# Kernel tuning notes

Measured on AMD Instinct MI355X. Metric: run time of the kernel, lower is better.

Reference implementation:

```python
import jax, jax.numpy as jnp
import numpy as np

I, C, H, W = 8, 32, 240, 320
GX = GY = GZ = 64


def setup_inputs() -> dict:
    key = jax.random.key(0)
    k_img, = jax.random.split(key, 1)
    images = jax.random.normal(k_img, (I, C, H, W), dtype=jnp.float32)

    # Camera intrinsics (shared across views)
    fx = fy = 300.0
    cx, cy = (W - 1) / 2.0, (H - 1) / 2.0
    K = jnp.array([[fx, 0.0, cx], [0.0, fy, cy], [0.0, 0.0, 1.0]], dtype=jnp.float32)

    # World->camera extrinsics: identity rotation, cameras spread along x
    centers = jnp.stack(
        [jnp.linspace(-0.175, 0.175, I), jnp.zeros(I), jnp.zeros(I)], axis=1
    ).astype(jnp.float32)  # [I,3] camera centers in world
    Rm = jnp.broadcast_to(jnp.eye(3, dtype=jnp.float32), (I, 3, 3))
    t = -jnp.einsum('iab,ib->ia', Rm, centers)  # t = -R c
    T_cw = jnp.concatenate(
        [jnp.concatenate([Rm, t[:, :, None]], axis=2),
         jnp.broadcast_to(jnp.array([[0.0, 0.0, 0.0, 1.0]], dtype=jnp.float32), (I, 1, 4))],
        axis=1,
    )  # [I,4,4]
    transformations = jnp.einsum('ab,ibc->iac', K, T_cw[:, :3, :])  # [I,3,4]

    # Voxel grid of world coordinates in front of the cameras
    xs = jnp.linspace(-1.0, 1.0, GX)
    ys = jnp.linspace(-1.0, 1.0, GY)
    zs = jnp.linspace(1.5, 3.5, GZ)
    gx, gy, gz = jnp.meshgrid(xs, ys, zs, indexing='ij')
    coordinates = jnp.stack([gx, gy, gz], axis=0).astype(jnp.float32)  # [3,X,Y,Z]

    return {
        'images': images,
        'transformations': transformations,
        'T_cw': T_cw,
        'coordinates': coordinates,
    }


def reference(images, transformations, T_cw, coordinates):
    # images: [I,C,H,W]; transformations: [I,3,4]; T_cw: [I,4,4]; coordinates: [3,X,Y,Z]
    Ii, Cc, Hh, Ww = images.shape
    X, Y, Z = coordinates.shape[1:]
    pts = coordinates.reshape(3, -1)  # [3, N]
    N = pts.shape[1]
    ph = jnp.concatenate([pts, jnp.ones((1, N), pts.dtype)], axis=0)  # [4, N]

    # Camera-frame depth
    cam = jnp.einsum('iab,bn->ian', T_cw[:, :3, :], ph)  # [I,3,N]
    depth = cam[:, 2, :]  # [I,N]

    # Pixel projection
    proj = jnp.einsum('iab,bn->ian', transformations, ph)  # [I,3,N]
    wz = proj[:, 2, :]
    wz_safe = jnp.where(jnp.abs(wz) < 1e-8, 1e-8, wz)
    u = proj[:, 0, :] / wz_safe
    v = proj[:, 1, :] / wz_safe

    valid = (u >= 0) & (u <= Ww - 1) & (v >= 0) & (v <= Hh - 1) & (depth > 0)
    validf = valid.astype(images.dtype)  # [I,N]

    # Nearest-neighbor grid sampling (grid_sampling_mode='nearest')
    ui = jnp.clip(jnp.round(u), 0, Ww - 1).astype(jnp.int32)
    vi = jnp.clip(jnp.round(v), 0, Hh - 1).astype(jnp.int32)
    feats = jax.vmap(lambda img, vv, uu: img[:, vv, uu])(images, vi, ui)  # [I,C,N]
    feats = feats * validf[:, None, :]

    # Viewing direction: normalized ray from camera center to voxel
    Rm = T_cw[:, :3, :3]
    t = T_cw[:, :3, 3]
    centers = -jnp.einsum('iba,ib->ia', Rm, t)  # R^T t -> camera centers [I,3]
    d = pts[None, :, :] - centers[:, :, None]  # [I,3,N]
    d = d / (jnp.linalg.norm(d, axis=1, keepdims=True) + 1e-8)

    # Concatenate channels: features + projected depth + validity + view dir
    grid = jnp.concatenate(
        [feats, depth[:, None, :], validf[:, None, :], d], axis=1
    )  # [I, C+5, N]
    grid = grid.reshape(Ii, Cc + 5, X, Y, Z)
    return grid, coordinates
```

## Files before the change

kernel.cpp:

```cpp
#include <hip/hip_runtime.h>
#include <stdint.h>


constexpr int I_ = 8;
constexpr int C_ = 32;
constexpr int H_ = 240;
constexpr int W_ = 320;
constexpr int HW_ = H_ * W_;
constexpr int N_ = 1 << 18;
constexpr int OUTC_ = 37;

constexpr int GZT    = 16;
constexpr int ROWF   = 328;
constexpr int ROWB   = ROWF * 4;
constexpr int STAGEB = GZT * ROWB;
constexpr int NCHUNK = 21;
constexpr int BUFF   = NCHUNK * 256;
constexpr uint32_t PLANEB = HW_ * 4;

typedef __attribute__((address_space(3))) uint8_t       as3_b;
typedef __attribute__((address_space(1))) const uint8_t as1_b;

struct Proj { float u, v, depth; bool valid; };

__device__ __forceinline__ Proj project(const float* __restrict__ P,
                                        const float* __restrict__ T,
                                        float x, float y, float z) {
    Proj r;
    r.depth = T[8]*x + T[9]*y + T[10]*z + T[11];
    const float px = P[0]*x + P[1]*y + P[2]*z  + P[3];
    const float py = P[4]*x + P[5]*y + P[6]*z  + P[7];
    const float pz = P[8]*x + P[9]*y + P[10]*z + P[11];
    const float wz = (fabsf(pz) < 1e-8f) ? 1e-8f : pz;
    r.u = px / wz;
    r.v = py / wz;
    r.valid = (r.u >= 0.0f) && (r.u <= (float)(W_-1)) &&
              (r.v >= 0.0f) && (r.v <= (float)(H_-1)) && (r.depth > 0.0f);
    return r;
}

__global__ __launch_bounds__(256) void smear_stage(
    const float* __restrict__ images,
    const float* __restrict__ trans,
    const float* __restrict__ T_cw,
    const float* __restrict__ coords,
    float* __restrict__ out)
{
    __shared__ float xs[64];
    __shared__ float zs[GZT];
    __shared__ float yv;
    __shared__ int   rowv[GZT];
    __shared__ alignas(16) float stagef[2][BUFF];

    const int cpx = (int)gridDim.x >> 3;
    const int bid = ((int)blockIdx.x & 7) * cpx + ((int)blockIdx.x >> 3);
    const int i  = bid >> 8;
    const int gy = (bid >> 2) & 63;
    const int zg = bid & 3;
    const int nbase = gy * 64 + zg * GZT;

    const int t = (int)threadIdx.x;
    const int w = t >> 6;
    const int lane = t & 63;

    if (t < 64)            xs[t]      = coords[(size_t)t * 4096 + nbase];
    else if (t < 64 + GZT) zs[t - 64] = coords[2 * N_ + nbase + (t - 64)];
    else if (t == 80)      yv         = coords[N_ + nbase];
    __syncthreads();

    const float* P = trans + i * 12;
    const float* T = T_cw + i * 16;
    const float y = yv;

    if (t < GZT) {
        Proj p0 = project(P, T, xs[0], y, zs[t]);
        rowv[t] = (int)fminf(fmaxf(rintf(p0.v), 0.0f), (float)(H_-1));
    }
    __syncthreads();

    const int gx = t >> 2;
    const int j0 = (t & 3) * 4;
    const float x = xs[gx];

    int   lofsf[4];
    float vf[4];
    int ok = 1;
    #pragma unroll
    for (int j = 0; j < 4; ++j) {
        const int s = j0 + j;
        Proj pr = project(P, T, x, y, zs[s]);
        const int ui = (int)fminf(fmaxf(rintf(pr.u), 0.0f), (float)(W_-1));
        const int vi = (int)fminf(fmaxf(rintf(pr.v), 0.0f), (float)(H_-1));
        vf[j]    = pr.valid ? 1.0f : 0.0f;
        lofsf[j] = s * ROWF + ui;
        ok &= ((vi == rowv[s]) || !pr.valid) ? 1 : 0;
    }
    const int blockok = __syncthreads_and(ok);

    float* optr = out + (size_t)i * OUTC_ * N_ + nbase + (size_t)gx * 4096 + j0;
    const uint8_t* img_i = (const uint8_t*)(images + (size_t)i * C_ * HW_);

    if (blockok) {
        uint32_t coff[6];
        #pragma unroll
        for (int q = 0; q < 6; ++q) {
            const int qg = w + 4 * q;
            coff[q] = 0;
            if (qg < NCHUNK) {
                const int p = qg * 1024 + lane * 16;
                int s = p / ROWB; if (s > GZT - 1) s = GZT - 1;
                const int off = p - s * ROWB;
                uint32_t ro = (uint32_t)(rowv[s] * (W_ * 4) + off);
                const uint32_t lim = PLANEB - 16;
                coff[q] = ro < lim ? ro : lim;
            }
        }

        #pragma unroll
        for (int q = 0; q < 6; ++q) {
            const int qg = w + 4 * q;
            if (qg < NCHUNK)
                __builtin_amdgcn_global_load_lds(
                    (const as1_b*)(img_i + coff[q]),
                    (as3_b*)&stagef[0][qg * 256], 16, 0, 0);
        }
        __syncthreads();

        float4 pend;
        for (int c = 0; c < C_; ++c) {
            if (c) *(float4*)(optr + (size_t)(c - 1) * N_) = pend;
            if (c + 1 < C_) {
                const uint8_t* plane = img_i + (size_t)(c + 1) * PLANEB;
                float* dstb = stagef[(c + 1) & 1];
                #pragma unroll
                for (int q = 0; q < 6; ++q) {
                    const int qg = w + 4 * q;
                    if (qg < NCHUNK)
                        __builtin_amdgcn_global_load_lds(
                            (const as1_b*)(plane + coff[q]),
                            (as3_b*)&dstb[qg * 256], 16, 0, 0);
                }
            }
            const float* bb = stagef[c & 1];
            const float g0 = bb[lofsf[0]] * vf[0];
            const float g1 = bb[lofsf[1]] * vf[1];
            const float g2 = bb[lofsf[2]] * vf[2];
            const float g3 = bb[lofsf[3]] * vf[3];
            pend = make_float4(g0, g1, g2, g3);
            __syncthreads();
        }
        *(float4*)(optr + (size_t)(C_ - 1) * N_) = pend;
    } else {
        for (int c = 0; c < C_; ++c) {
            const float* plane = (const float*)img_i + (size_t)c * HW_;
            float g[4];
            #pragma unroll
            for (int j = 0; j < 4; ++j) {
                const int s = j0 + j;
                Proj pr = project(P, T, x, y, zs[s]);
                const int ui = (int)fminf(fmaxf(rintf(pr.u), 0.0f), (float)(W_-1));
                const int vi = (int)fminf(fmaxf(rintf(pr.v), 0.0f), (float)(H_-1));
                g[j] = pr.valid ? plane[vi * W_ + ui] : 0.0f;
            }
            *(float4*)(optr + (size_t)c * N_) = make_float4(g[0], g[1], g[2], g[3]);
        }
    }

    const float cxx = -(T[0]*T[3] + T[4]*T[7] + T[8] *T[11]);
    const float cyy = -(T[1]*T[3] + T[5]*T[7] + T[9] *T[11]);
    const float czz = -(T[2]*T[3] + T[6]*T[7] + T[10]*T[11]);
    float dep[4], dxn[4], dyn[4], dzn[4];
    #pragma unroll
    for (int j = 0; j < 4; ++j) {
        const int s = j0 + j;
        const float z = zs[s];
        Proj pr = project(P, T, x, y, z);
        dep[j] = pr.depth;
        vf[j]  = pr.valid ? 1.0f : 0.0f;
        const float dx = x - cxx, dy = y - cyy, dz = z - czz;
        const float inv = 1.0f / (sqrtf(dx*dx + dy*dy + dz*dz) + 1e-8f);
        dxn[j] = dx * inv; dyn[j] = dy * inv; dzn[j] = dz * inv;
    }
    *(float4*)(optr + (size_t)32 * N_) = make_float4(dep[0], dep[1], dep[2], dep[3]);
    *(float4*)(optr + (size_t)33 * N_) = make_float4(vf[0],  vf[1],  vf[2],  vf[3]);
    *(float4*)(optr + (size_t)34 * N_) = make_float4(dxn[0], dxn[1], dxn[2], dxn[3]);
    *(float4*)(optr + (size_t)35 * N_) = make_float4(dyn[0], dyn[1], dyn[2], dyn[3]);
    *(float4*)(optr + (size_t)36 * N_) = make_float4(dzn[0], dzn[1], dzn[2], dzn[3]);
}

extern "C" void kernel_launch(void* const* d_in, const int* in_sizes, int n_in,
                              void* d_out, int out_size, void* d_ws, size_t ws_size,
                              hipStream_t stream) {
    const float* images = (const float*)d_in[0];
    const float* trans  = (const float*)d_in[1];
    const float* T_cw   = (const float*)d_in[2];
    const float* coords = (const float*)d_in[3];
    float* out = (float*)d_out;

    smear_stage<<<I_ * 64 * 4, 256, 0, stream>>>(images, trans, T_cw, coords, out);

    float* coords_out = out + (size_t)I_ * OUTC_ * N_;
    hipMemcpyAsync(coords_out, coords, (size_t)3 * N_ * sizeof(float),
                   hipMemcpyDeviceToDevice, stream);
}
```

Baseline: 482.4 us.

## Split channels into groups across blocks and use nontemporal output stores

Each block now handles 8 of the 32 channels, so the grid grows fourfold. This adds parallelism and shortens each block's serial channel loop. The block-to-view mapping changes so that consecutive blocks cover different views, which is likely aimed at XCD/L2 locality. Output stores become nontemporal to avoid cache pollution. The trade-off is that projection setup and the row-check are repeated in each channel group. The depth, validity and view-direction channels are written only by group 0.

```diff
diff --git a/kernel.cpp b/kernel.cpp
--- a/kernel.cpp
+++ b/kernel.cpp
@@ -4,22 +4,29 @@
 
 constexpr int I_ = 8;
 constexpr int C_ = 32;
+constexpr int W_ = 320;
 constexpr int H_ = 240;
-constexpr int W_ = 320;
 constexpr int HW_ = H_ * W_;
 constexpr int N_ = 1 << 18;
 constexpr int OUTC_ = 37;
+constexpr int CPG_ = 8;
+constexpr int NCG_ = C_ / CPG_;
 
 constexpr int GZT    = 16;
 constexpr int ROWF   = 328;
 constexpr int ROWB   = ROWF * 4;
-constexpr int STAGEB = GZT * ROWB;
 constexpr int NCHUNK = 21;
 constexpr int BUFF   = NCHUNK * 256;
 constexpr uint32_t PLANEB = HW_ * 4;
 
 typedef __attribute__((address_space(3))) uint8_t       as3_b;
 typedef __attribute__((address_space(1))) const uint8_t as1_b;
+typedef float f32x4 __attribute__((ext_vector_type(4)));
+
+__device__ __forceinline__ void ntstore4(float* p, float a, float b, float c, float d) {
+    f32x4 v = {a, b, c, d};
+    __builtin_nontemporal_store(v, (f32x4*)p);
+}
 
 struct Proj { float u, v, depth; bool valid; };
 
@@ -52,11 +59,13 @@
     __shared__ int   rowv[GZT];
     __shared__ alignas(16) float stagef[2][BUFF];
 
-    const int cpx = (int)gridDim.x >> 3;
-    const int bid = ((int)blockIdx.x & 7) * cpx + ((int)blockIdx.x >> 3);
-    const int i  = bid >> 8;
-    const int gy = (bid >> 2) & 63;
-    const int zg = bid & 3;
+    const int i       = (int)blockIdx.x & 7;
+    const int pos     = (int)blockIdx.x >> 3;
+    const int cg      = pos >> 8;
+    const int spatial = pos & 255;
+    const int gy = spatial >> 2;
+    const int zg = spatial & 3;
+    const int cb = cg * CPG_;
     const int nbase = gy * 64 + zg * GZT;
 
     const int t = (int)threadIdx.x;
@@ -116,21 +125,24 @@
             }
         }
 
-        #pragma unroll
-        for (int q = 0; q < 6; ++q) {
-            const int qg = w + 4 * q;
-            if (qg < NCHUNK)
-                __builtin_amdgcn_global_load_lds(
-                    (const as1_b*)(img_i + coff[q]),
-                    (as3_b*)&stagef[0][qg * 256], 16, 0, 0);
+        {
+            const uint8_t* plane = img_i + (size_t)cb * PLANEB;
+            #pragma unroll
+            for (int q = 0; q < 6; ++q) {
+                const int qg = w + 4 * q;
+                if (qg < NCHUNK)
+                    __builtin_amdgcn_global_load_lds(
+                        (const as1_b*)(plane + coff[q]),
+                        (as3_b*)&stagef[0][qg * 256], 16, 0, 0);
+            }
         }
         __syncthreads();
 
-        float4 pend;
-        for (int c = 0; c < C_; ++c) {
-            if (c) *(float4*)(optr + (size_t)(c - 1) * N_) = pend;
-            if (c + 1 < C_) {
-                const uint8_t* plane = img_i + (size_t)(c + 1) * PLANEB;
+        float g0, g1, g2, g3;
+        for (int c = 0; c < CPG_; ++c) {
+            if (c) ntstore4(optr + (size_t)(cb + c - 1) * N_, g0, g1, g2, g3);
+            if (c + 1 < CPG_) {
+                const uint8_t* plane = img_i + (size_t)(cb + c + 1) * PLANEB;
                 float* dstb = stagef[(c + 1) & 1];
                 #pragma unroll
                 for (int q = 0; q < 6; ++q) {
@@ -142,17 +154,16 @@
                 }
             }
             const float* bb = stagef[c & 1];
-            const float g0 = bb[lofsf[0]] * vf[0];
-            const float g1 = bb[lofsf[1]] * vf[1];
-            const float g2 = bb[lofsf[2]] * vf[2];
-            const float g3 = bb[lofsf[3]] * vf[3];
-            pend = make_float4(g0, g1, g2, g3);
+            g0 = bb[lofsf[0]] * vf[0];
+            g1 = bb[lofsf[1]] * vf[1];
+            g2 = bb[lofsf[2]] * vf[2];
+            g3 = bb[lofsf[3]] * vf[3];
             __syncthreads();
         }
-        *(float4*)(optr + (size_t)(C_ - 1) * N_) = pend;
+        ntstore4(optr + (size_t)(cb + CPG_ - 1) * N_, g0, g1, g2, g3);
     } else {
-        for (int c = 0; c < C_; ++c) {
-            const float* plane = (const float*)img_i + (size_t)c * HW_;
+        for (int c = 0; c < CPG_; ++c) {
+            const float* plane = (const float*)img_i + (size_t)(cb + c) * HW_;
             float g[4];
             #pragma unroll
             for (int j = 0; j < 4; ++j) {
@@ -162,30 +173,32 @@
                 const int vi = (int)fminf(fmaxf(rintf(pr.v), 0.0f), (float)(H_-1));
                 g[j] = pr.valid ? plane[vi * W_ + ui] : 0.0f;
             }
-            *(float4*)(optr + (size_t)c * N_) = make_float4(g[0], g[1], g[2], g[3]);
-        }
-    }
-
-    const float cxx = -(T[0]*T[3] + T[4]*T[7] + T[8] *T[11]);
-    const float cyy = -(T[1]*T[3] + T[5]*T[7] + T[9] *T[11]);
-    const float czz = -(T[2]*T[3] + T[6]*T[7] + T[10]*T[11]);
-    float dep[4], dxn[4], dyn[4], dzn[4];
-    #pragma unroll
-    for (int j = 0; j < 4; ++j) {
-        const int s = j0 + j;
-        const float z = zs[s];
-        Proj pr = project(P, T, x, y, z);
-        dep[j] = pr.depth;
-        vf[j]  = pr.valid ? 1.0f : 0.0f;
-        const float dx = x - cxx, dy = y - cyy, dz = z - czz;
-        const float inv = 1.0f / (sqrtf(dx*dx + dy*dy + dz*dz) + 1e-8f);
-        dxn[j] = dx * inv; dyn[j] = dy * inv; dzn[j] = dz * inv;
-    }
-    *(float4*)(optr + (size_t)32 * N_) = make_float4(dep[0], dep[1], dep[2], dep[3]);
-    *(float4*)(optr + (size_t)33 * N_) = make_float4(vf[0],  vf[1],  vf[2],  vf[3]);
-    *(float4*)(optr + (size_t)34 * N_) = make_float4(dxn[0], dxn[1], dxn[2], dxn[3]);
-    *(float4*)(optr + (size_t)35 * N_) = make_float4(dyn[0], dyn[1], dyn[2], dyn[3]);
-    *(float4*)(optr + (size_t)36 * N_) = make_float4(dzn[0], dzn[1], dzn[2], dzn[3]);
+            ntstore4(optr + (size_t)(cb + c) * N_, g[0], g[1], g[2], g[3]);
+        }
+    }
+
+    if (cg == 0) {
+        const float cxx = -(T[0]*T[3] + T[4]*T[7] + T[8] *T[11]);
+        const float cyy = -(T[1]*T[3] + T[5]*T[7] + T[9] *T[11]);
+        const float czz = -(T[2]*T[3] + T[6]*T[7] + T[10]*T[11]);
+        float dep[4], dxn[4], dyn[4], dzn[4];
+        #pragma unroll
+        for (int j = 0; j < 4; ++j) {
+            const int s = j0 + j;
+            const float z = zs[s];
+            Proj pr = project(P, T, x, y, z);
+            dep[j] = pr.depth;
+            vf[j]  = pr.valid ? 1.0f : 0.0f;
+            const float dx = x - cxx, dy = y - cyy, dz = z - czz;
+            const float inv = 1.0f / (sqrtf(dx*dx + dy*dy + dz*dz) + 1e-8f);
+            dxn[j] = dx * inv; dyn[j] = dy * inv; dzn[j] = dz * inv;
+        }
+        ntstore4(optr + (size_t)32 * N_, dep[0], dep[1], dep[2], dep[3]);
+        ntstore4(optr + (size_t)33 * N_, vf[0],  vf[1],  vf[2],  vf[3]);
+        ntstore4(optr + (size_t)34 * N_, dxn[0], dxn[1], dxn[2], dxn[3]);
+        ntstore4(optr + (size_t)35 * N_, dyn[0], dyn[1], dyn[2], dyn[3]);
+        ntstore4(optr + (size_t)36 * N_, dzn[0], dzn[1], dzn[2], dzn[3]);
+    }
 }
 
 extern "C" void kernel_launch(void* const* d_in, const int* in_sizes, int n_in,
@@ -197,7 +210,7 @@
     const float* coords = (const float*)d_in[3];
     float* out = (float*)d_out;
 
-    smear_stage<<<I_ * 64 * 4, 256, 0, stream>>>(images, trans, T_cw, coords, out);
+    smear_stage<<<I_ * NCG_ * 64 * 4, 256, 0, stream>>>(images, trans, T_cw, coords, out);
 
     float* coords_out = out + (size_t)I_ * OUTC_ * N_;
     hipMemcpyAsync(coords_out, coords, (size_t)3 * N_ * sizeof(float),
```

Result: faster. 472.9 us (-2.0%).
